# Optimization experiments

Hardware: AMD Instinct MI355X
Metric: run time of the kernel (lower is better)

Reference implementation:

```python
import jax, jax.numpy as jnp
import numpy as np

T = 4096          # total packed tokens (4 docs x 1024)
NUM_DOCS = 4
H = 16            # n_heads
D = 64            # head_dim == v_head_dim
TOPK = 64         # per-token top-k KV selection (<= min doc len)


def setup_inputs() -> dict:
    key = jax.random.key(0)
    kq, kk, kv, ki, ks = jax.random.split(key, 5)
    q = jax.random.normal(kq, (T, H, D), dtype=jnp.float32)
    k = jax.random.normal(kk, (T, H, D), dtype=jnp.float32)
    v = jax.random.normal(kv, (T, H, D), dtype=jnp.float32)
    # 4 equal-length documents of 1024 tokens
    cu_seqlens = (jnp.arange(NUM_DOCS + 1, dtype=jnp.int32) * (T // NUM_DOCS))
    # global top-k indices; reference clamps them into the owning document
    topk_indices = jax.random.randint(ki, (T, TOPK), 0, T, dtype=jnp.int32)
    # selector scores in (0,1), like indexer softmax outputs
    topk_scores = jax.random.uniform(ks, (T, TOPK), dtype=jnp.float32)
    return {
        "q_packed": q,
        "k_packed": k,
        "v_packed": v,
        "cu_seqlens": cu_seqlens,
        "topk_indices": topk_indices,
        "topk_scores": topk_scores,
    }


def reference(q_packed, k_packed, v_packed, cu_seqlens, topk_indices, topk_scores):
    total_tokens, n_heads, head_dim = q_packed.shape
    scale = head_dim ** -0.5

    # Per-token document assignment (vectorized replacement for the doc loop).
    tok = jnp.arange(total_tokens, dtype=cu_seqlens.dtype)
    seg = jnp.searchsorted(cu_seqlens[1:], tok, side="right")  # (T,) doc id
    start = cu_seqlens[seg]                                    # (T,)
    seq_len = cu_seqlens[seg + 1] - start                      # (T,)

    # Localize and clamp top-k indices into the owning document, then
    # convert back to global packed indices for gathering.
    local = jnp.clip(topk_indices - start[:, None], 0, (seq_len - 1)[:, None])
    gidx = start[:, None] + local                              # (T, K)

    k_gathered = k_packed[gidx]   # (T, K, H, D)
    v_gathered = v_packed[gidx]   # (T, K, H, D)

    # q . k_sel, softmax over the k selected keys
    scores = jnp.einsum("thd,tkhd->thk", q_packed, k_gathered) * scale
    w = jax.nn.softmax(scores, axis=-1)                        # (T, H, K)

    # Modulate by selector scores (head-shared) and renormalize.
    w = w * topk_scores[:, None, :]
    w = w / (jnp.sum(w, axis=-1, keepdims=True) + 1e-12)

    out = jnp.einsum("thk,tkhd->thd", w, v_gathered)           # (T, H, D)
    return out
```

## Files before the change

### kernel.cpp

```cpp
#include <hip/hip_runtime.h>
#include <hip/hip_fp16.h>


#define T_TOK 4096
#define NH    16
#define HD    64
#define KSEL  64
#define KV_ELEMS (T_TOK * NH * HD)

typedef _Float16 h2v __attribute__((ext_vector_type(2)));

static __device__ __forceinline__ h2v u2h2v(unsigned u) {
    return __builtin_bit_cast(h2v, u);
}
static __device__ __forceinline__ __half2 u2h2(unsigned u) {
    return __builtin_bit_cast(__half2, u);
}
static __device__ __forceinline__ h2v f2h2v(float a, float b) {
    __half2 t = __floats2half2_rn(a, b);
    return __builtin_bit_cast(h2v, t);
}

template<int CTRL>
static __device__ __forceinline__ float dpp_addf(float x) {
    const int s = __builtin_amdgcn_update_dpp(
        0, __builtin_bit_cast(int, x), CTRL, 0xF, 0xF, true);
    return x + __builtin_bit_cast(float, s);
}

template<int IMM>
static __device__ __forceinline__ float swz_addf(float x) {
    const int s = __builtin_amdgcn_ds_swizzle(__builtin_bit_cast(int, x), IMM);
    return x + __builtin_bit_cast(float, s);
}
template<int IMM>
static __device__ __forceinline__ __half2 swz_hadd2(__half2 x) {
    const int s = __builtin_amdgcn_ds_swizzle(__builtin_bit_cast(int, x), IMM);
    return __hadd2(x, __builtin_bit_cast(__half2, s));
}
static __device__ __forceinline__ __half2 sh32_hadd2(__half2 x) {
    const int s = __shfl_xor(__builtin_bit_cast(int, x), 32, 64);
    return __hadd2(x, __builtin_bit_cast(__half2, s));
}

__global__ __launch_bounds__(256) void cvt_fp16(
    const float4* __restrict__ kM, const float4* __restrict__ vM,
    uint2* __restrict__ kH, uint2* __restrict__ vH)
{
    const int n4 = KV_ELEMS / 4;
    const int i  = blockIdx.x * blockDim.x + threadIdx.x;
    const bool isK = i < n4;
    const float4 f = isK ? kM[i] : vM[i - n4];
    __half2 lo = __floats2half2_rn(f.x, f.y);
    __half2 hi = __floats2half2_rn(f.z, f.w);
    uint2 u;
    u.x = __builtin_bit_cast(unsigned, lo);
    u.y = __builtin_bit_cast(unsigned, hi);
    if (isK) kH[i] = u; else vH[i - n4] = u;
}

__global__ __launch_bounds__(256) void dsa_sparse_attn(
    const float*  __restrict__ qM,
    const __half* __restrict__ kH,
    const __half* __restrict__ vH,
    const int*    __restrict__ cu,
    const int*    __restrict__ tidx,
    const float*  __restrict__ tsc,
    float*        __restrict__ out,
    int num_docs)
{
    const int wave = threadIdx.x >> 6;
    const int lane = threadIdx.x & 63;

    const int b            = blockIdx.x;
    const int xcd          = b & 7;
    const int j            = b >> 3;
    const int token_block  = j & 255;
    const int slice_within = j >> 8;
    const int s            = xcd + (slice_within << 3);
    const int h            = s & (NH - 1);
    const int t            = (s >> 4) * (T_TOK / 4) + token_block * 4 + wave;
    const int gid          = t * NH + h;

    int seg = 0;
    for (int i = 1; i < num_docs; ++i)
        if (t >= cu[i]) seg = i;
    const int start = cu[seg];
    const int len   = cu[seg + 1] - start;

    int idx = tidx[t * KSEL + lane];
    int loc = idx - start;
    loc = loc < 0 ? 0 : loc;
    loc = loc > len - 1 ? len - 1 : loc;
    const int g = start + loc;

    const int laneQ8 = lane >> 3;
    const int laneC8 = lane & 7;

    const float4* qv = (const float4*)(qM + gid * HD);
    const float4 fA = qv[laneC8 * 2];
    const float4 fB = qv[laneC8 * 2 + 1];
    const h2v q0 = f2h2v(fA.x, fA.y);
    const h2v q1 = f2h2v(fA.z, fA.w);
    const h2v q2 = f2h2v(fB.x, fB.y);
    const h2v q3 = f2h2v(fB.z, fB.w);

    const uint4* kf = (const uint4*)kH;
    const uint4* vf = (const uint4*)vH;
    const float* scb = tsc + t * KSEL;

    float S2part = 0.f;
    __half2 acc0 = u2h2(0u), acc1 = u2h2(0u), acc2 = u2h2(0u), acc3 = u2h2(0u);

    #pragma unroll
    for (int rg = 0; rg < 8; ++rg) {
        const int row = rg * 8 + laneQ8;
        const int gr  = __shfl(g, row, 64);
        const int base = (gr * NH + h) * 8 + laneC8;
        const uint4 kk = kf[base];
        const uint4 vv = vf[base];
        const float sck = scb[row];

        float p = 0.f;
        p = __builtin_amdgcn_fdot2(u2h2v(kk.x), q0, p, false);
        p = __builtin_amdgcn_fdot2(u2h2v(kk.y), q1, p, false);
        p = __builtin_amdgcn_fdot2(u2h2v(kk.z), q2, p, false);
        p = __builtin_amdgcn_fdot2(u2h2v(kk.w), q3, p, false);
        p = dpp_addf<0xB1>(p);
        p = dpp_addf<0x4E>(p);
        p = dpp_addf<0x141>(p);

        const float w = __expf(p * 0.125f) * sck;
        S2part += w;
        const __half2 w2 = __floats2half2_rn(w, w);
        acc0 = __hfma2(w2, u2h2(vv.x), acc0);
        acc1 = __hfma2(w2, u2h2(vv.y), acc1);
        acc2 = __hfma2(w2, u2h2(vv.z), acc2);
        acc3 = __hfma2(w2, u2h2(vv.w), acc3);
    }

    float S2 = S2part;
    S2 = dpp_addf<0x140>(S2);
    S2 = swz_addf<0x401F>(S2);
    S2 += __shfl_xor(S2, 32, 64);

    acc0 = swz_hadd2<0x201F>(acc0); acc1 = swz_hadd2<0x201F>(acc1);
    acc2 = swz_hadd2<0x201F>(acc2); acc3 = swz_hadd2<0x201F>(acc3);
    acc0 = swz_hadd2<0x401F>(acc0); acc1 = swz_hadd2<0x401F>(acc1);
    acc2 = swz_hadd2<0x401F>(acc2); acc3 = swz_hadd2<0x401F>(acc3);
    acc0 = sh32_hadd2(acc0); acc1 = sh32_hadd2(acc1);
    acc2 = sh32_hadd2(acc2); acc3 = sh32_hadd2(acc3);

    if (laneQ8 == 0) {
        const float inv = __builtin_amdgcn_rcpf(S2);
        const float2 a0 = __half22float2(acc0);
        const float2 a1 = __half22float2(acc1);
        const float2 a2 = __half22float2(acc2);
        const float2 a3 = __half22float2(acc3);
        float4* op = (float4*)(out + gid * HD + laneC8 * 8);
        op[0] = make_float4(a0.x * inv, a0.y * inv, a1.x * inv, a1.y * inv);
        op[1] = make_float4(a2.x * inv, a2.y * inv, a3.x * inv, a3.y * inv);
    }
}

extern "C" void kernel_launch(void* const* d_in, const int* in_sizes, int n_in,
                              void* d_out, int out_size, void* d_ws, size_t ws_size,
                              hipStream_t stream) {
    const float* q   = (const float*)d_in[0];
    const float* k   = (const float*)d_in[1];
    const float* v   = (const float*)d_in[2];
    const int*   cu  = (const int*)d_in[3];
    const int*   ti  = (const int*)d_in[4];
    const float* ts  = (const float*)d_in[5];
    float*       out = (float*)d_out;
    const int num_docs = in_sizes[3] - 1;

    __half* kH = (__half*)d_ws;
    __half* vH = kH + KV_ELEMS;

    const int n4 = KV_ELEMS / 4;
    hipLaunchKernelGGL(cvt_fp16, dim3(2 * n4 / 256), dim3(256), 0, stream,
                       (const float4*)k, (const float4*)v,
                       (uint2*)kH, (uint2*)vH);

    const int total_waves = T_TOK * NH;
    hipLaunchKernelGGL(dsa_sparse_attn, dim3(total_waves / 4), dim3(256), 0,
                       stream, q, (const __half*)kH, (const __half*)vH,
                       cu, ti, ts, out, num_docs);
}
```

Measured before the change: 144.3 us.

## Compute QK scores with MFMA and stage weights through shared memory

```diff
diff --git a/kernel.cpp b/kernel.cpp
--- a/kernel.cpp
+++ b/kernel.cpp
@@ -8,26 +8,21 @@
 #define KSEL  64
 #define KV_ELEMS (T_TOK * NH * HD)
 
-typedef _Float16 h2v __attribute__((ext_vector_type(2)));
-
-static __device__ __forceinline__ h2v u2h2v(unsigned u) {
-    return __builtin_bit_cast(h2v, u);
-}
+typedef _Float16 h8 __attribute__((ext_vector_type(8)));
+typedef float    f4v __attribute__((ext_vector_type(4)));
+
 static __device__ __forceinline__ __half2 u2h2(unsigned u) {
     return __builtin_bit_cast(__half2, u);
 }
-static __device__ __forceinline__ h2v f2h2v(float a, float b) {
-    __half2 t = __floats2half2_rn(a, b);
-    return __builtin_bit_cast(h2v, t);
-}
-
+static __device__ __forceinline__ unsigned h22u(__half2 h) {
+    return __builtin_bit_cast(unsigned, h);
+}
 template<int CTRL>
 static __device__ __forceinline__ float dpp_addf(float x) {
     const int s = __builtin_amdgcn_update_dpp(
         0, __builtin_bit_cast(int, x), CTRL, 0xF, 0xF, true);
     return x + __builtin_bit_cast(float, s);
 }
-
 template<int IMM>
 static __device__ __forceinline__ float swz_addf(float x) {
     const int s = __builtin_amdgcn_ds_swizzle(__builtin_bit_cast(int, x), IMM);
@@ -51,11 +46,9 @@
     const int i  = blockIdx.x * blockDim.x + threadIdx.x;
     const bool isK = i < n4;
     const float4 f = isK ? kM[i] : vM[i - n4];
-    __half2 lo = __floats2half2_rn(f.x, f.y);
-    __half2 hi = __floats2half2_rn(f.z, f.w);
     uint2 u;
-    u.x = __builtin_bit_cast(unsigned, lo);
-    u.y = __builtin_bit_cast(unsigned, hi);
+    u.x = h22u(__floats2half2_rn(f.x, f.y));
+    u.y = h22u(__floats2half2_rn(f.z, f.w));
     if (isK) kH[i] = u; else vH[i - n4] = u;
 }
 
@@ -69,6 +62,8 @@
     float*        __restrict__ out,
     int num_docs)
 {
+    __shared__ uint2 s_wg[4][64];
+
     const int wave = threadIdx.x >> 6;
     const int lane = threadIdx.x & 63;
 
@@ -88,61 +83,92 @@
     const int start = cu[seg];
     const int len   = cu[seg + 1] - start;
 
-    int idx = tidx[t * KSEL + lane];
-    int loc = idx - start;
-    loc = loc < 0 ? 0 : loc;
-    loc = loc > len - 1 ? len - 1 : loc;
+    int loc = tidx[t * KSEL + lane] - start;
+    loc = loc < 0 ? 0 : (loc > len - 1 ? len - 1 : loc);
     const int g = start + loc;
+    const float sc = tsc[t * KSEL + lane];
+
+    const int quad = lane >> 4;
+
+    const uint4* kf = (const uint4*)kH;
+    uint4 a1[4], a2[4];
+    #pragma unroll
+    for (int g4 = 0; g4 < 4; ++g4) {
+        const int gr = __shfl(g, g4 * 16 + (lane & 15), 64);
+        const int base = (gr * NH + h) * 8 + quad;
+        a1[g4] = kf[base];
+        a2[g4] = kf[base + 4];
+    }
+    const float* qrow = qM + gid * HD;
+    const float4 qa = *(const float4*)(qrow + quad * 8);
+    const float4 qb = *(const float4*)(qrow + quad * 8 + 4);
+    const float4 qc = *(const float4*)(qrow + 32 + quad * 8);
+    const float4 qd = *(const float4*)(qrow + 32 + quad * 8 + 4);
+    uint4 qu1, qu2;
+    qu1.x = h22u(__floats2half2_rn(qa.x, qa.y));
+    qu1.y = h22u(__floats2half2_rn(qa.z, qa.w));
+    qu1.z = h22u(__floats2half2_rn(qb.x, qb.y));
+    qu1.w = h22u(__floats2half2_rn(qb.z, qb.w));
+    qu2.x = h22u(__floats2half2_rn(qc.x, qc.y));
+    qu2.y = h22u(__floats2half2_rn(qc.z, qc.w));
+    qu2.z = h22u(__floats2half2_rn(qd.x, qd.y));
+    qu2.w = h22u(__floats2half2_rn(qd.z, qd.w));
+    const h8 qb1 = __builtin_bit_cast(h8, qu1);
+    const h8 qb2 = __builtin_bit_cast(h8, qu2);
+
+    f4v D[4];
+    #pragma unroll
+    for (int g4 = 0; g4 < 4; ++g4) {
+        f4v d = {0.f, 0.f, 0.f, 0.f};
+        d = __builtin_amdgcn_mfma_f32_16x16x32_f16(
+                __builtin_bit_cast(h8, a1[g4]), qb1, d, 0, 0, 0);
+        d = __builtin_amdgcn_mfma_f32_16x16x32_f16(
+                __builtin_bit_cast(h8, a2[g4]), qb2, d, 0, 0, 0);
+        D[g4] = d;
+    }
+
+    float S2;
+    {
+        const f4v Ta = ((lane >> 2) & 1) ? D[1] : D[0];
+        const f4v Tb = ((lane >> 2) & 1) ? D[3] : D[2];
+        const f4v Tg = ((lane >> 3) & 1) ? Tb : Ta;
+        const float va  = (lane & 1) ? Tg.y : Tg.x;
+        const float vb  = (lane & 1) ? Tg.w : Tg.z;
+        const float sv  = (lane & 2) ? vb : va;
+        const int roww = 16 * ((lane >> 2) & 3) + 4 * quad + (lane & 3);
+        const float scr = __shfl(sc, roww, 64);
+        const int   grw = __shfl(g,  roww, 64);
+        const float w = __expf(sv * 0.125f) * scr;
+        uint2 wg;
+        wg.x = h22u(__floats2half2_rn(w, w));
+        wg.y = (unsigned)grw;
+        s_wg[wave][roww] = wg;
+        float r = w;
+        r = dpp_addf<0xB1>(r);
+        r = dpp_addf<0x4E>(r);
+        r = dpp_addf<0x141>(r);
+        r = dpp_addf<0x140>(r);
+        r = swz_addf<0x401F>(r);
+        r += __shfl_xor(r, 32, 64);
+        S2 = r;
+    }
 
     const int laneQ8 = lane >> 3;
     const int laneC8 = lane & 7;
-
-    const float4* qv = (const float4*)(qM + gid * HD);
-    const float4 fA = qv[laneC8 * 2];
-    const float4 fB = qv[laneC8 * 2 + 1];
-    const h2v q0 = f2h2v(fA.x, fA.y);
-    const h2v q1 = f2h2v(fA.z, fA.w);
-    const h2v q2 = f2h2v(fB.x, fB.y);
-    const h2v q3 = f2h2v(fB.z, fB.w);
-
-    const uint4* kf = (const uint4*)kH;
     const uint4* vf = (const uint4*)vH;
-    const float* scb = tsc + t * KSEL;
-
-    float S2part = 0.f;
+
     __half2 acc0 = u2h2(0u), acc1 = u2h2(0u), acc2 = u2h2(0u), acc3 = u2h2(0u);
-
     #pragma unroll
     for (int rg = 0; rg < 8; ++rg) {
-        const int row = rg * 8 + laneQ8;
-        const int gr  = __shfl(g, row, 64);
-        const int base = (gr * NH + h) * 8 + laneC8;
-        const uint4 kk = kf[base];
-        const uint4 vv = vf[base];
-        const float sck = scb[row];
-
-        float p = 0.f;
-        p = __builtin_amdgcn_fdot2(u2h2v(kk.x), q0, p, false);
-        p = __builtin_amdgcn_fdot2(u2h2v(kk.y), q1, p, false);
-        p = __builtin_amdgcn_fdot2(u2h2v(kk.z), q2, p, false);
-        p = __builtin_amdgcn_fdot2(u2h2v(kk.w), q3, p, false);
-        p = dpp_addf<0xB1>(p);
-        p = dpp_addf<0x4E>(p);
-        p = dpp_addf<0x141>(p);
-
-        const float w = __expf(p * 0.125f) * sck;
-        S2part += w;
-        const __half2 w2 = __floats2half2_rn(w, w);
+        const uint2 wg = s_wg[wave][rg * 8 + laneQ8];
+        const __half2 w2 = u2h2(wg.x);
+        const int gv = (int)wg.y;
+        const uint4 vv = vf[(gv * NH + h) * 8 + laneC8];
         acc0 = __hfma2(w2, u2h2(vv.x), acc0);
         acc1 = __hfma2(w2, u2h2(vv.y), acc1);
         acc2 = __hfma2(w2, u2h2(vv.z), acc2);
         acc3 = __hfma2(w2, u2h2(vv.w), acc3);
     }
-
-    float S2 = S2part;
-    S2 = dpp_addf<0x140>(S2);
-    S2 = swz_addf<0x401F>(S2);
-    S2 += __shfl_xor(S2, 32, 64);
 
     acc0 = swz_hadd2<0x201F>(acc0); acc1 = swz_hadd2<0x201F>(acc1);
     acc2 = swz_hadd2<0x201F>(acc2); acc3 = swz_hadd2<0x201F>(acc3);
@@ -154,12 +180,12 @@
     if (laneQ8 == 0) {
         const float inv = __builtin_amdgcn_rcpf(S2);
         const float2 a0 = __half22float2(acc0);
-        const float2 a1 = __half22float2(acc1);
-        const float2 a2 = __half22float2(acc2);
-        const float2 a3 = __half22float2(acc3);
+        const float2 a1f = __half22float2(acc1);
+        const float2 a2f = __half22float2(acc2);
+        const float2 a3f = __half22float2(acc3);
         float4* op = (float4*)(out + gid * HD + laneC8 * 8);
-        op[0] = make_float4(a0.x * inv, a0.y * inv, a1.x * inv, a1.y * inv);
-        op[1] = make_float4(a2.x * inv, a2.y * inv, a3.x * inv, a3.y * inv);
+        op[0] = make_float4(a0.x * inv, a0.y * inv, a1f.x * inv, a1f.y * inv);
+        op[1] = make_float4(a2f.x * inv, a2f.y * inv, a3f.x * inv, a3f.y * inv);
     }
 }
 
```

Measured after the change: 160.0 us. +10.9%, slower.
